# Optimization experiments

Measured on AMD Instinct MI355X. Metric: run time of the kernel, lower is better.

The kernel has to match this reference:

```python
import jax, jax.numpy as jnp
import numpy as np

B, S, D, H = 2, 512, 1024, 8
DK = D // H
DFF = 4 * D
R = 51
SEP = 64


def setup_inputs() -> dict:
    key = jax.random.key(0)
    ks = jax.random.split(key, 12)
    def w(k, shape, scale=0.02):
        return jax.random.normal(k, shape, jnp.float32) * scale
    return {
        "x": jax.random.normal(ks[0], (B, S, D), jnp.float32),
        "relation": jax.random.randint(ks[1], (B, S, S), 0, R),
        "mask": jnp.ones((B, S, S), jnp.int32),
        "sep_id": SEP,
        "history_reg": jnp.ones((1,), jnp.float32),
        "Wq": w(ks[2], (D, D)), "bq": jnp.zeros((D,), jnp.float32),
        "Wk": w(ks[3], (D, D)), "bk": jnp.zeros((D,), jnp.float32),
        "Wv": w(ks[4], (D, D)), "bv": jnp.zeros((D,), jnp.float32),
        "Wo": w(ks[5], (D, D)), "bo": jnp.zeros((D,), jnp.float32),
        "rel_k_emb": w(ks[6], (R, DK)),
        "rel_v_emb": w(ks[7], (R, DK)),
        "ln1_g": jnp.ones((D,), jnp.float32), "ln1_b": jnp.zeros((D,), jnp.float32),
        "ln2_g": jnp.ones((D,), jnp.float32), "ln2_b": jnp.zeros((D,), jnp.float32),
        "W1": w(ks[8], (D, DFF)), "b1": jnp.zeros((DFF,), jnp.float32),
        "W2": w(ks[9], (DFF, D)), "b2": jnp.zeros((D,), jnp.float32),
    }


def _layer_norm(x, g, b, eps=1e-5):
    m = jnp.mean(x, axis=-1, keepdims=True)
    v = jnp.mean(jnp.square(x - m), axis=-1, keepdims=True)
    return (x - m) * jax.lax.rsqrt(v + eps) * g + b


def _forward(x, relation, mask, sep_id, history_reg, Wq, bq, Wk, bk, Wv, bv, Wo, bo,
             rel_k_emb, rel_v_emb, ln1_g, ln1_b, ln2_g, ln2_b, W1, b1, W2, b2):
    b, s, d = x.shape
    # relation-aware self-attention sublayer (pre-norm)
    h = _layer_norm(x, ln1_g, ln1_b)
    rk = rel_k_emb[relation]  # [B,S,S,DK]
    rv = rel_v_emb[relation]  # [B,S,S,DK]
    def proj(W, bias):
        return (h @ W + bias).reshape(b, s, H, DK).transpose(0, 2, 1, 3)  # [B,H,S,DK]
    q, k, v = proj(Wq, bq), proj(Wk, bk), proj(Wv, bv)
    scores = jnp.einsum("bhid,bhjd->bhij", q, k) + jnp.einsum("bhid,bijd->bhij", q, rk)
    scores = scores / jnp.sqrt(jnp.float32(DK))
    scores = jnp.where(mask[:, None, :, :] == 0, jnp.float32(-1e9), scores)
    attn = jax.nn.softmax(scores, axis=-1)  # [B,H,S,S]
    ctx = jnp.einsum("bhij,bhjd->bhid", attn, v) + jnp.einsum("bhij,bijd->bhid", attn, rv)
    ctx = ctx.transpose(0, 2, 1, 3).reshape(b, s, d)
    attn_out = ctx @ Wo + bo
    # history regularization loss: attention mass on history tokens (positions < sep_id)
    loss = history_reg[0] * jnp.mean(attn[:, :, :, :sep_id])
    x = x + attn_out
    # FFN sublayer (pre-norm)
    h2 = _layer_norm(x, ln2_g, ln2_b)
    ffn = jax.nn.relu(h2 @ W1 + b1) @ W2 + b2
    x = x + ffn
    return x, loss


def reference(x, relation, mask, sep_id, history_reg, Wq, bq, Wk, bk, Wv, bv, Wo, bo,
              rel_k_emb, rel_v_emb, ln1_g, ln1_b, ln2_g, ln2_b, W1, b1, W2, b2):
    return _forward(x, relation, mask, sep_id, history_reg, Wq, bq, Wk, bk, Wv, bv,
                    Wo, bo, rel_k_emb, rel_v_emb, ln1_g, ln1_b, ln2_g, ln2_b,
                    W1, b1, W2, b2)
```

## Files before the change

### kernel.cpp

```cpp
#include <hip/hip_runtime.h>
#include <hip/hip_bf16.h>

#define NB 2
#define NS 512
#define ND 1024
#define NH 8
#define NDK 128
#define NDFF 4096
#define RPAD 64
#define BSROWS 1024
#define NBH 16
#define QT 16
#define SLB 536

typedef __bf16 bf16x8 __attribute__((ext_vector_type(8)));
typedef __bf16 bf16x4 __attribute__((ext_vector_type(4)));
typedef float f32x4 __attribute__((ext_vector_type(4)));

#define BM 64
#define BN 64
#define BK 64

__device__ __forceinline__ void gload16(const void* g, void* l) {
    __builtin_amdgcn_global_load_lds(
        (const __attribute__((address_space(1))) void*)g,
        (__attribute__((address_space(3))) void*)l, 16, 0, 0);
}

__global__ __launch_bounds__(256, 4) void gemm64(
    const __bf16* __restrict__ A, const __bf16* __restrict__ Bt,
    __bf16* __restrict__ vt,
    float* __restrict__ Cf, __bf16* __restrict__ Cb,
    const float* __restrict__ bias,
    int Ksp, int lda, int ldb, int ldc,
    long sA, long sA2, int zdivA,
    long sB, long sB2, int zdivB,
    long sC, int nsplit, long sPart, int flags)
{
    __shared__ __bf16 As0[BM * BK];
    __shared__ __bf16 As1[BM * BK];
    __shared__ __bf16 Bs0[BN * BK];
    __shared__ __bf16 Bs1[BN * BK];

    const unsigned gx = gridDim.x, gy = gridDim.y;
    const unsigned n = gx * gy * gridDim.z;
    const unsigned o = blockIdx.x + gx * (blockIdx.y + gy * blockIdx.z);
    const unsigned q = n >> 3, r = n & 7, xcd = o & 7;
    const unsigned nl = (xcd < r ? xcd * (q + 1) : r * (q + 1) + (xcd - r) * q) + (o >> 3);
    const unsigned bx = nl % gx, tmp = nl / gx;
    const unsigned by = tmp % gy, bz = tmp / gy;

    const int z = bz;
    const int bh = z / nsplit, sp = z - bh * nsplit;
    const long kbase = (long)sp * Ksp;
    A  += (long)(bh / zdivA) * sA + (long)(bh % zdivA) * sA2 + kbase;
    Bt += (long)(bh / zdivB) * sB + (long)(bh % zdivB) * sB2 + kbase;
    const long cbase = (long)bh * sC + (long)sp * sPart;

    const int tM = by * BM, tN = bx * BN;
    const int t = threadIdx.x, lane = t & 63, w = t >> 6;
    const int wr = w >> 1, wc = w & 1;

    const int srow = lane >> 3;
    const int scolE = ((((lane & 7) << 4) ^ (srow << 4)) >> 1);

    const __bf16* gA = A + (long)(tM + srow) * lda + scolE;
    const __bf16* gB = Bt + (long)(tN + srow) * ldb + scolE;

    f32x4 acc[2][2];
#pragma unroll
    for (int m = 0; m < 2; ++m)
#pragma unroll
        for (int nn = 0; nn < 2; ++nn)
#pragma unroll
            for (int j = 0; j < 4; ++j) acc[m][nn][j] = 0.f;

    const int r16 = lane & 15;
    const int kq = (lane >> 4) * 8;
    const int xorE = (r16 & 7) * 8;
    const int nt = Ksp / BK;

    auto STAGE = [&](__bf16* as, __bf16* bs, int k0) {
#pragma unroll
        for (int i = 0; i < 2; ++i) {
            const int rr = (w + i * 4) * 8;
            gload16(gA + (long)rr * lda + k0, (void*)&as[rr * BK]);
            gload16(gB + (long)rr * ldb + k0, (void*)&bs[rr * BK]);
        }
    };
    auto COMPUTE = [&](const __bf16* as, const __bf16* bs) {
        __builtin_amdgcn_s_setprio(1);
#pragma unroll
        for (int ks = 0; ks < 2; ++ks) {
            bf16x8 af[2], bv[2];
#pragma unroll
            for (int m = 0; m < 2; ++m)
                af[m] = *(const bf16x8*)&as[(wr * 32 + m * 16 + r16) * BK + ((ks * 32 + kq) ^ xorE)];
#pragma unroll
            for (int nn = 0; nn < 2; ++nn)
                bv[nn] = *(const bf16x8*)&bs[(wc * 32 + nn * 16 + r16) * BK + ((ks * 32 + kq) ^ xorE)];
#pragma unroll
            for (int m = 0; m < 2; ++m)
#pragma unroll
                for (int nn = 0; nn < 2; ++nn)
                    acc[m][nn] = __builtin_amdgcn_mfma_f32_16x16x32_bf16(af[m], bv[nn], acc[m][nn], 0, 0, 0);
        }
        __builtin_amdgcn_s_setprio(0);
    };

    STAGE(As0, Bs0, 0);
    STAGE(As1, Bs1, BK);
    for (int tt = 0; tt < nt; tt += 2) {
        asm volatile("s_waitcnt vmcnt(4)\n\ts_barrier" ::: "memory");
        COMPUTE(As0, Bs0);
        asm volatile("s_waitcnt lgkmcnt(0)\n\ts_barrier" ::: "memory");
        const bool more = (tt + 2 < nt);
        if (more) {
            STAGE(As0, Bs0, (tt + 2) * BK);
            asm volatile("s_waitcnt vmcnt(4)\n\ts_barrier" ::: "memory");
        } else {
            asm volatile("s_waitcnt vmcnt(0)\n\ts_barrier" ::: "memory");
        }
        COMPUTE(As1, Bs1);
        asm volatile("s_waitcnt lgkmcnt(0)\n\ts_barrier" ::: "memory");
        if (more) STAGE(As1, Bs1, (tt + 3) * BK);
    }

    const bool relu = (flags & 1) != 0;
    const bool vmode = (flags & 8) && (tN >= 2 * ND);
#pragma unroll
    for (int m = 0; m < 2; ++m) {
        const int gr0 = tM + wr * 32 + m * 16 + (lane >> 4) * 4;
#pragma unroll
        for (int nn = 0; nn < 2; ++nn) {
            const int gc = tN + wc * 32 + nn * 16 + (lane & 15);
            const float bb = bias ? bias[gc] : 0.f;
            if (vmode) {
                const int hd = gc - 2 * ND;
                const int b = gr0 >> 9, i = gr0 & 511;
                bf16x4 ov;
#pragma unroll
                for (int j = 0; j < 4; ++j) ov[j] = (__bf16)(acc[m][nn][j] + bb);
                *(bf16x4*)&vt[(((long)b * NH + (hd >> 7)) * NDK + (hd & 127)) * NS + i] = ov;
            } else {
#pragma unroll
                for (int j = 0; j < 4; ++j) {
                    float v = acc[m][nn][j] + bb;
                    if (relu) v = fmaxf(v, 0.f);
                    const long idx = cbase + (long)(gr0 + j) * ldc + gc;
                    if (Cb) Cb[idx] = (__bf16)v;
                    else Cf[idx] = v;
                }
            }
        }
    }
}

__global__ __launch_bounds__(256, 2) void attn_fused(
    const __bf16* __restrict__ qkvb, const __bf16* __restrict__ vt,
    const __bf16* __restrict__ relkT, const __bf16* __restrict__ relvT,
    const int* __restrict__ relation, const int* __restrict__ mask,
    __bf16* __restrict__ ctxm, float* __restrict__ loss_part,
    const int* __restrict__ sep_p)
{
    __shared__ __bf16 Sl[QT * SLB];
    __shared__ __bf16 Ks0[64 * NDK];
    __shared__ __bf16 Ks1[64 * NDK];
    __shared__ float qrl[QT][RPAD];
    __shared__ float bins[QT][68];
    __shared__ float redl[4];

    const unsigned o = blockIdx.x + 32u * blockIdx.y;
    const unsigned nl = (o & 7) * 64u + (o >> 3);
    const int qt = nl & 31, bh = nl >> 5;
    const int b = bh >> 3, h = bh & 7;
    const int i0 = qt * QT;

    const int t = threadIdx.x, lane = t & 63, w = t >> 6;
    const int r16 = lane & 15;
    const int kq = (lane >> 4) * 8;
    const int xorE = (r16 & 7) * 8;
    const int sep = *sep_p;

    bf16x8 qf[4];
    {
        const __bf16* qrow = qkvb + ((long)(b * NS + i0 + r16)) * (3 * ND) + h * NDK;
#pragma unroll
        for (int ks = 0; ks < 4; ++ks)
            qf[ks] = *(const bf16x8*)(qrow + ks * 32 + kq);
    }

    int4 ra[4][2], ma[4][2];
#pragma unroll
    for (int rr = 0; rr < 4; ++rr) {
        const long rg = (long)(b * NS + i0 + w * 4 + rr) * NS;
        ra[rr][0] = ((const int4*)(relation + rg))[lane * 2];
        ra[rr][1] = ((const int4*)(relation + rg))[lane * 2 + 1];
        ma[rr][0] = ((const int4*)(mask + rg))[lane * 2];
        ma[rr][1] = ((const int4*)(mask + rg))[lane * 2 + 1];
    }

    {
        f32x4 a;
#pragma unroll
        for (int j = 0; j < 4; ++j) a[j] = 0.f;
#pragma unroll
        for (int ks = 0; ks < 4; ++ks) {
            const bf16x8 bfr = *(const bf16x8*)(relkT + (long)(w * 16 + r16) * NDK + ks * 32 + kq);
            a = __builtin_amdgcn_mfma_f32_16x16x32_bf16(qf[ks], bfr, a, 0, 0, 0);
        }
#pragma unroll
        for (int j = 0; j < 4; ++j)
            qrl[(lane >> 4) * 4 + j][w * 16 + (lane & 15)] = a[j];
    }
    for (int idx = t; idx < QT * 68; idx += 256) ((float*)bins)[idx] = 0.f;

    auto KSTAGE = [&](__bf16* ksb, int kv0) {
#pragma unroll
        for (int ii = 0; ii < 4; ++ii) {
            const int Lc = (w * 4 + ii) * 64 + lane;
            const int j = Lc >> 4, cc = Lc & 15;
            gload16(qkvb + ((long)(b * NS + kv0 + j)) * (3 * ND) + ND + h * NDK + ((cc ^ (j & 7)) << 3),
                    (void*)&ksb[(w * 4 + ii) * 512]);
        }
    };
    auto SCOMP = [&](const __bf16* ksb, int kv0) {
        f32x4 s;
#pragma unroll
        for (int j = 0; j < 4; ++j) s[j] = 0.f;
#pragma unroll
        for (int ks = 0; ks < 4; ++ks) {
            const bf16x8 bfr = *(const bf16x8*)&ksb[(w * 16 + r16) * NDK + ((ks * 32 + kq) ^ xorE)];
            s = __builtin_amdgcn_mfma_f32_16x16x32_bf16(qf[ks], bfr, s, 0, 0, 0);
        }
        const int colb = kv0 + w * 16 + (lane & 15);
#pragma unroll
        for (int j = 0; j < 4; ++j)
            Sl[((lane >> 4) * 4 + j) * SLB + colb] = (__bf16)s[j];
    };

    KSTAGE(Ks0, 0);
    KSTAGE(Ks1, 64);
    for (int tt = 0; tt < 8; tt += 2) {
        asm volatile("s_waitcnt vmcnt(4)\n\ts_barrier" ::: "memory");
        SCOMP(Ks0, tt * 64);
        asm volatile("s_waitcnt lgkmcnt(0)\n\ts_barrier" ::: "memory");
        const bool more = (tt + 2 < 8);
        if (more) {
            KSTAGE(Ks0, (tt + 2) * 64);
            asm volatile("s_waitcnt vmcnt(4)\n\ts_barrier" ::: "memory");
        } else {
            asm volatile("s_waitcnt vmcnt(0)\n\ts_barrier" ::: "memory");
        }
        SCOMP(Ks1, (tt + 1) * 64);
        asm volatile("s_waitcnt lgkmcnt(0)\n\ts_barrier" ::: "memory");
        if (more) KSTAGE(Ks1, (tt + 3) * 64);
    }

    const int brow = t & 15;
    const int bj0 = (t >> 4) * 32;
    int4 br[8];
    {
        const int4* rp = (const int4*)(relation + ((long)(b * NS + i0 + brow)) * NS + bj0);
#pragma unroll
        for (int c = 0; c < 8; ++c) br[c] = rp[c];
    }

    auto VSTAGE = [&](__bf16* vs, int kv0) {
#pragma unroll
        for (int ii = 0; ii < 4; ++ii) {
            const int d = w * 32 + ii * 8 + (lane >> 3);
            const int cc = lane & 7;
            gload16(vt + ((long)bh * NDK + d) * NS + kv0 + ((cc ^ (d & 7)) << 3),
                    (void*)&vs[(w * 32 + ii * 8) * 64]);
        }
    };
    VSTAGE(Ks0, 0);
    VSTAGE(Ks1, 64);

    const float sc = 0.088388347648318447f;
    float lsum = 0.f;
#pragma unroll
    for (int rr = 0; rr < 4; ++rr) {
        const int row = w * 4 + rr;
        const bf16x8 sv = *(const bf16x8*)&Sl[row * SLB + lane * 8];
        int rl[8], mm[8];
        rl[0] = ra[rr][0].x; rl[1] = ra[rr][0].y; rl[2] = ra[rr][0].z; rl[3] = ra[rr][0].w;
        rl[4] = ra[rr][1].x; rl[5] = ra[rr][1].y; rl[6] = ra[rr][1].z; rl[7] = ra[rr][1].w;
        mm[0] = ma[rr][0].x; mm[1] = ma[rr][0].y; mm[2] = ma[rr][0].z; mm[3] = ma[rr][0].w;
        mm[4] = ma[rr][1].x; mm[5] = ma[rr][1].y; mm[6] = ma[rr][1].z; mm[7] = ma[rr][1].w;
        float v[8];
        float mx = -1e30f;
#pragma unroll
        for (int q = 0; q < 8; ++q) {
            float vv = ((float)sv[q] + qrl[row][rl[q]]) * sc;
            if (mm[q] == 0) vv = -1e9f;
            v[q] = vv;
            mx = fmaxf(mx, vv);
        }
#pragma unroll
        for (int of = 32; of > 0; of >>= 1) mx = fmaxf(mx, __shfl_xor(mx, of, 64));
        float sm = 0.f;
#pragma unroll
        for (int q = 0; q < 8; ++q) { v[q] = __expf(v[q] - mx); sm += v[q]; }
#pragma unroll
        for (int of = 32; of > 0; of >>= 1) sm += __shfl_xor(sm, of, 64);
        const float inv = 1.f / sm;
        bf16x8 av;
#pragma unroll
        for (int q = 0; q < 8; ++q) {
            const float a = v[q] * inv;
            av[q] = (__bf16)a;
            if (lane * 8 + q < sep) lsum += a;
        }
        *(bf16x8*)&Sl[row * SLB + lane * 8] = av;
    }
#pragma unroll
    for (int of = 32; of > 0; of >>= 1) lsum += __shfl_xor(lsum, of, 64);
    if (lane == 0) redl[w] = lsum;
    asm volatile("s_waitcnt lgkmcnt(0)\n\ts_barrier" ::: "memory");
    if (t == 0) loss_part[bh * 32 + qt] = redl[0] + redl[1] + redl[2] + redl[3];

    {
        const __bf16* ap = &Sl[brow * SLB + bj0];
#pragma unroll
        for (int c = 0; c < 8; ++c) {
            const bf16x4 a4 = *(const bf16x4*)(ap + c * 4);
            atomicAdd(&bins[brow][br[c].x], (float)a4[0]);
            atomicAdd(&bins[brow][br[c].y], (float)a4[1]);
            atomicAdd(&bins[brow][br[c].z], (float)a4[2]);
            atomicAdd(&bins[brow][br[c].w], (float)a4[3]);
        }
    }

    f32x4 oacc[2];
#pragma unroll
    for (int nn = 0; nn < 2; ++nn)
#pragma unroll
        for (int j = 0; j < 4; ++j) oacc[nn][j] = 0.f;

    auto PVCOMP = [&](const __bf16* vs, int kv0) {
        __builtin_amdgcn_s_setprio(1);
#pragma unroll
        for (int ks = 0; ks < 2; ++ks) {
            const bf16x8 af = *(const bf16x8*)&Sl[r16 * SLB + kv0 + ks * 32 + kq];
#pragma unroll
            for (int nn = 0; nn < 2; ++nn) {
                const bf16x8 bv = *(const bf16x8*)&vs[(w * 32 + nn * 16 + r16) * 64 + ((ks * 32 + kq) ^ xorE)];
                oacc[nn] = __builtin_amdgcn_mfma_f32_16x16x32_bf16(af, bv, oacc[nn], 0, 0, 0);
            }
        }
        __builtin_amdgcn_s_setprio(0);
    };

    for (int tt = 0; tt < 8; tt += 2) {
        asm volatile("s_waitcnt vmcnt(4)\n\ts_barrier" ::: "memory");
        PVCOMP(Ks0, tt * 64);
        asm volatile("s_waitcnt lgkmcnt(0)\n\ts_barrier" ::: "memory");
        const bool more = (tt + 2 < 8);
        if (more) {
            VSTAGE(Ks0, (tt + 2) * 64);
            asm volatile("s_waitcnt vmcnt(4)\n\ts_barrier" ::: "memory");
        } else {
            asm volatile("s_waitcnt vmcnt(0)\n\ts_barrier" ::: "memory");
        }
        PVCOMP(Ks1, (tt + 1) * 64);
        asm volatile("s_waitcnt lgkmcnt(0)\n\ts_barrier" ::: "memory");
        if (more) VSTAGE(Ks1, (tt + 3) * 64);
    }

#pragma unroll
    for (int kc = 0; kc < 2; ++kc) {
        const float4 b0 = *(const float4*)&bins[r16][kc * 32 + kq];
        const float4 b1 = *(const float4*)&bins[r16][kc * 32 + kq + 4];
        bf16x8 af;
        af[0] = (__bf16)b0.x; af[1] = (__bf16)b0.y; af[2] = (__bf16)b0.z; af[3] = (__bf16)b0.w;
        af[4] = (__bf16)b1.x; af[5] = (__bf16)b1.y; af[6] = (__bf16)b1.z; af[7] = (__bf16)b1.w;
#pragma unroll
        for (int nn = 0; nn < 2; ++nn) {
            const bf16x8 bfr = *(const bf16x8*)(relvT + (long)(w * 32 + nn * 16 + r16) * RPAD + kc * 32 + kq);
            oacc[nn] = __builtin_amdgcn_mfma_f32_16x16x32_bf16(af, bfr, oacc[nn], 0, 0, 0);
        }
    }
#pragma unroll
    for (int nn = 0; nn < 2; ++nn)
#pragma unroll
        for (int j = 0; j < 4; ++j) {
            const int row = (lane >> 4) * 4 + j;
            ctxm[((long)(b * NS + i0 + row)) * ND + h * NDK + w * 32 + nn * 16 + (lane & 15)] =
                (__bf16)oacc[nn][j];
        }
}

__global__ void prep_weights(
    const float* __restrict__ Wq, const float* __restrict__ Wk,
    const float* __restrict__ Wv, const float* __restrict__ Wo,
    const float* __restrict__ W1, const float* __restrict__ W2,
    const float* __restrict__ relv,
    const float* __restrict__ bq, const float* __restrict__ bk,
    const float* __restrict__ bv, const float* __restrict__ relk,
    const float* __restrict__ x, const float* __restrict__ ln1g,
    const float* __restrict__ ln1b,
    __bf16* __restrict__ WqkvT, __bf16* __restrict__ WoT,
    __bf16* __restrict__ W1T, __bf16* __restrict__ W2T,
    __bf16* __restrict__ relvT, float* __restrict__ biasqkv,
    __bf16* __restrict__ relkT, __bf16* __restrict__ h1, int R)
{
    const int tile = blockIdx.x;
    const int t = threadIdx.y * 32 + threadIdx.x;

    if (tile >= 12372) {
        const long row = tile - 12372;
        const float* xr = x + row * ND;
        float4 v = reinterpret_cast<const float4*>(xr)[t];
        float s = v.x + v.y + v.z + v.w;
        float s2 = v.x * v.x + v.y * v.y + v.z * v.z + v.w * v.w;
#pragma unroll
        for (int o = 32; o > 0; o >>= 1) {
            s += __shfl_xor(s, o, 64);
            s2 += __shfl_xor(s2, o, 64);
        }
        __shared__ float red[8];
        const int lane = t & 63, wv = t >> 6;
        if (lane == 0) { red[wv] = s; red[4 + wv] = s2; }
        __syncthreads();
        s = red[0] + red[1] + red[2] + red[3];
        s2 = red[4] + red[5] + red[6] + red[7];
        const float mean = s * (1.f / ND);
        const float var = s2 * (1.f / ND) - mean * mean;
        const float rs = rsqrtf(var + 1e-5f);
        const float xv[4] = {v.x, v.y, v.z, v.w};
        bf16x4 o;
#pragma unroll
        for (int j = 0; j < 4; ++j) {
            const int c = t * 4 + j;
            o[j] = (__bf16)((xv[j] - mean) * rs * ln1g[c] + ln1b[c]);
        }
        *(bf16x4*)&h1[row * ND + t * 4] = o;
        return;
    }
    if (tile >= 12296) {
        const int ft = (tile - 12296) * 256 + t;
        if (ft < ND) biasqkv[ft] = bq[ft];
        else if (ft < 2 * ND) biasqkv[ft] = bk[ft - ND];
        else if (ft < 3 * ND) biasqkv[ft] = bv[ft - 2 * ND];
        else {
            const int idx = ft - 3 * ND;
            if (idx < 128 * NDK) {
                const int r = idx / NDK;
                relkT[idx] = (r < R) ? (__bf16)relk[idx] : (__bf16)0.f;
            }
        }
        return;
    }
    const float* src; __bf16* dst;
    int rows_in, cols_in, ldo, kx, ny;
    if (tile < 4096) {
        const int m = tile >> 10, r = tile & 1023;
        kx = r & 31; ny = r >> 5;
        rows_in = 1024; cols_in = 1024; ldo = 1024;
        src = m == 0 ? Wq : m == 1 ? Wk : m == 2 ? Wv : Wo;
        dst = m == 3 ? WoT : WqkvT + (size_t)m * 1024 * 1024;
    } else if (tile < 8192) {
        const int r = tile - 4096;
        kx = r & 31; ny = r >> 5;
        rows_in = 1024; cols_in = 4096; ldo = 1024; src = W1; dst = W1T;
    } else if (tile < 12288) {
        const int r = tile - 8192;
        kx = r & 127; ny = r >> 7;
        rows_in = 4096; cols_in = 1024; ldo = 4096; src = W2; dst = W2T;
    } else {
        const int r = tile - 12288;
        kx = r & 1; ny = r >> 1;
        rows_in = R; cols_in = 128; ldo = 64; src = relv; dst = relvT;
    }

    __shared__ float tl[32][33];
    const int k0 = kx * 32, n0 = ny * 32;
    const int tx = threadIdx.x, ty = threadIdx.y;
#pragma unroll
    for (int dy = 0; dy < 32; dy += 8) {
        const int k = k0 + ty + dy, nn = n0 + tx;
        tl[ty + dy][tx] = (k < rows_in && nn < cols_in) ? src[(long)k * cols_in + nn] : 0.f;
    }
    __syncthreads();
#pragma unroll
    for (int dy = 0; dy < 32; dy += 8) {
        const int nn = n0 + ty + dy, k = k0 + tx;
        if (nn < cols_in && k < ldo) dst[(long)nn * ldo + k] = (__bf16)tl[tx][ty + dy];
    }
}

__global__ __launch_bounds__(256) void wo_reduce_ln(
    const float* __restrict__ P, const float* __restrict__ x,
    const float* __restrict__ bo, const float* __restrict__ g,
    const float* __restrict__ bb, float* __restrict__ out,
    __bf16* __restrict__ h2)
{
    const int row = blockIdx.x;
    const int t = threadIdx.x;
    const long i4 = (long)row * 256 + t;
    const long sP = (long)BSROWS * ND / 4;
    const float4* P4 = (const float4*)P;
    float4 s = P4[i4];
    const float4 t1 = P4[i4 + sP];
    s.x += t1.x; s.y += t1.y; s.z += t1.z; s.w += t1.w;
    const int col = t * 4;
    const float4 xv = ((const float4*)x)[i4];
    const float4 bv = *(const float4*)&bo[col];
    float4 o;
    o.x = s.x + xv.x + bv.x; o.y = s.y + xv.y + bv.y;
    o.z = s.z + xv.z + bv.z; o.w = s.w + xv.w + bv.w;
    ((float4*)out)[i4] = o;

    float sum = o.x + o.y + o.z + o.w;
    float sum2 = o.x * o.x + o.y * o.y + o.z * o.z + o.w * o.w;
#pragma unroll
    for (int of = 32; of > 0; of >>= 1) {
        sum += __shfl_xor(sum, of, 64);
        sum2 += __shfl_xor(sum2, of, 64);
    }
    __shared__ float red[8];
    const int lane = t & 63, wv = t >> 6;
    if (lane == 0) { red[wv] = sum; red[4 + wv] = sum2; }
    __syncthreads();
    sum = red[0] + red[1] + red[2] + red[3];
    sum2 = red[4] + red[5] + red[6] + red[7];
    const float mean = sum * (1.f / ND);
    const float var = sum2 * (1.f / ND) - mean * mean;
    const float rs = rsqrtf(var + 1e-5f);
    const float ov[4] = {o.x, o.y, o.z, o.w};
    bf16x4 hb;
#pragma unroll
    for (int j = 0; j < 4; ++j)
        hb[j] = (__bf16)((ov[j] - mean) * rs * g[col + j] + bb[col + j]);
    *(bf16x4*)&h2[(long)row * ND + col] = hb;
}

__global__ __launch_bounds__(256) void ffn2_reduce(
    const float* __restrict__ P, const float* __restrict__ b2, float* __restrict__ out,
    const float* __restrict__ loss_part, const float* __restrict__ hist,
    const int* __restrict__ sep_p, float* __restrict__ out_loss)
{
    const int i4 = blockIdx.x * 256 + threadIdx.x;
    const long sP = (long)BSROWS * ND / 4;
    const float4* P4 = (const float4*)P;
    float4 s = P4[i4];
    const float4 t1 = P4[i4 + sP];
    s.x += t1.x; s.y += t1.y; s.z += t1.z; s.w += t1.w;
    const int col = (i4 * 4) & (ND - 1);
    const float4 bv = *(const float4*)&b2[col];
    float4 o = ((float4*)out)[i4];
    o.x += s.x + bv.x; o.y += s.y + bv.y;
    o.z += s.z + bv.z; o.w += s.w + bv.w;
    ((float4*)out)[i4] = o;

    if (blockIdx.x == 0) {
        const int t = threadIdx.x;
        float ls = 0.f;
        if (t < 128) {
            const float4 v = ((const float4*)loss_part)[t];
            ls = v.x + v.y + v.z + v.w;
        }
#pragma unroll
        for (int of = 32; of > 0; of >>= 1) ls += __shfl_xor(ls, of, 64);
        __shared__ float red[4];
        if ((t & 63) == 0) red[t >> 6] = ls;
        __syncthreads();
        if (t == 0) {
            const int sep = *sep_p;
            const float total = red[0] + red[1] + red[2] + red[3];
            const float denom = (float)NB * NH * NS * (float)(sep > 0 ? sep : 1);
            out_loss[0] = (sep > 0) ? hist[0] * total / denom : 0.f;
        }
    }
}

extern "C" void kernel_launch(void* const* d_in, const int* in_sizes, int n_in,
                              void* d_out, int out_size, void* d_ws, size_t ws_size,
                              hipStream_t stream)
{
    const float* x      = (const float*)d_in[0];
    const int* relation = (const int*)d_in[1];
    const int* mask     = (const int*)d_in[2];
    const int* sep_p    = (const int*)d_in[3];
    const float* hist   = (const float*)d_in[4];
    const float* Wq = (const float*)d_in[5],  *bq = (const float*)d_in[6];
    const float* Wk = (const float*)d_in[7],  *bk = (const float*)d_in[8];
    const float* Wv = (const float*)d_in[9],  *bv = (const float*)d_in[10];
    const float* Wo = (const float*)d_in[11], *bo = (const float*)d_in[12];
    const float* relk = (const float*)d_in[13];
    const float* relv = (const float*)d_in[14];
    const float* ln1g = (const float*)d_in[15], *ln1b = (const float*)d_in[16];
    const float* ln2g = (const float*)d_in[17], *ln2b = (const float*)d_in[18];
    const float* W1 = (const float*)d_in[19], *b1 = (const float*)d_in[20];
    const float* W2 = (const float*)d_in[21], *b2 = (const float*)d_in[22];
    const int R = in_sizes[13] / NDK;

    float* out = (float*)d_out;
    float* out_loss = out + (long)BSROWS * ND;

    char* p = (char*)d_ws;
    auto alloc = [&](size_t bytes) -> void* {
        void* r = (void*)p;
        p += (bytes + 255) & ~(size_t)255;
        return r;
    };
    __bf16* WqkvT   = (__bf16*)alloc((size_t)3 * ND * ND * 2);
    __bf16* WoT     = (__bf16*)alloc((size_t)ND * ND * 2);
    __bf16* W1T     = (__bf16*)alloc((size_t)NDFF * ND * 2);
    __bf16* W2T     = (__bf16*)alloc((size_t)ND * NDFF * 2);
    __bf16* relkT   = (__bf16*)alloc((size_t)128 * NDK * 2);
    __bf16* relvT   = (__bf16*)alloc((size_t)NDK * RPAD * 2);
    float*  biasqkv = (float*)alloc((size_t)3 * ND * 4);
    __bf16* h1      = (__bf16*)alloc((size_t)BSROWS * ND * 2);
    __bf16* qkvb    = (__bf16*)alloc((size_t)BSROWS * 3 * ND * 2);
    __bf16* vt      = (__bf16*)alloc((size_t)NBH * NDK * NS * 2);
    __bf16* ctxm    = (__bf16*)alloc((size_t)BSROWS * ND * 2);
    __bf16* h2      = (__bf16*)alloc((size_t)BSROWS * ND * 2);
    __bf16* F1      = (__bf16*)alloc((size_t)BSROWS * NDFF * 2);
    float*  loss_part = (float*)alloc((size_t)512 * 4);
    float*  arena   = (float*)alloc((size_t)16 * 1024 * 1024);
    float* woPart   = arena;
    float* f2Part   = arena + (size_t)2 * 1024 * 1024;

    const dim3 tb(32, 8);
    prep_weights<<<13396, tb, 0, stream>>>(Wq, Wk, Wv, Wo, W1, W2, relv,
                                           bq, bk, bv, relk, x, ln1g, ln1b,
                                           WqkvT, WoT, W1T, W2T, relvT,
                                           biasqkv, relkT, h1, R);

    gemm64<<<dim3(48, 16, 1), 256, 0, stream>>>(
        h1, WqkvT, vt, nullptr, qkvb, biasqkv,
        ND, ND, ND, 3 * ND,
        0, 0, 1, 0, 0, 1, 0, 1, 0, 8);

    attn_fused<<<dim3(32, 16), 256, 0, stream>>>(
        qkvb, vt, relkT, relvT, relation, mask, ctxm, loss_part, sep_p);

    gemm64<<<dim3(16, 16, 2), 256, 0, stream>>>(
        ctxm, WoT, nullptr, woPart, nullptr, nullptr,
        512, ND, ND, ND,
        0, 0, 1, 0, 0, 1,
        0, 2, (long)BSROWS * ND, 0);

    wo_reduce_ln<<<BSROWS, 256, 0, stream>>>(woPart, x, bo, ln2g, ln2b, out, h2);

    gemm64<<<dim3(64, 16, 1), 256, 0, stream>>>(
        h2, W1T, nullptr, nullptr, F1, b1,
        ND, ND, ND, NDFF,
        0, 0, 1, 0, 0, 1, 0, 1, 0, 1);

    gemm64<<<dim3(16, 16, 2), 256, 0, stream>>>(
        F1, W2T, nullptr, f2Part, nullptr, nullptr,
        2048, NDFF, NDFF, ND,
        0, 0, 1, 0, 0, 1,
        0, 2, (long)BSROWS * ND, 0);

    ffn2_reduce<<<1024, 256, 0, stream>>>(f2Part, b2, out,
                                          loss_part, hist, sep_p, out_loss);
}
```

Baseline: 131.6 us.

## Halve attention query tile to 8 rows and single-buffer K/V staging for occupancy

Shrinks the attention query tile from 16 to 8 rows, so twice as many blocks are launched (1024). K and V staging drops from double to single buffering to cut LDS use, and launch bounds are raised to 4 waves per SIMD. The aim is more resident blocks to hide latency. The cost is that half the MFMA rows are wasted on padding, K/V tiles are reloaded twice as often overall, and the prefetch overlap between load and compute is lost.

```diff
diff --git a/kernel.cpp b/kernel.cpp
--- a/kernel.cpp
+++ b/kernel.cpp
@@ -10,7 +10,7 @@
 #define RPAD 64
 #define BSROWS 1024
 #define NBH 16
-#define QT 16
+#define QT 8
 #define SLB 536
 
 typedef __bf16 bf16x8 __attribute__((ext_vector_type(8)));
@@ -156,7 +156,7 @@
     }
 }
 
-__global__ __launch_bounds__(256, 2) void attn_fused(
+__global__ __launch_bounds__(256, 4) void attn_fused(
     const __bf16* __restrict__ qkvb, const __bf16* __restrict__ vt,
     const __bf16* __restrict__ relkT, const __bf16* __restrict__ relvT,
     const int* __restrict__ relation, const int* __restrict__ mask,
@@ -164,42 +164,51 @@
     const int* __restrict__ sep_p)
 {
     __shared__ __bf16 Sl[QT * SLB];
-    __shared__ __bf16 Ks0[64 * NDK];
-    __shared__ __bf16 Ks1[64 * NDK];
+    __shared__ __bf16 Ks[64 * NDK];
     __shared__ float qrl[QT][RPAD];
     __shared__ float bins[QT][68];
     __shared__ float redl[4];
 
-    const unsigned o = blockIdx.x + 32u * blockIdx.y;
-    const unsigned nl = (o & 7) * 64u + (o >> 3);
-    const int qt = nl & 31, bh = nl >> 5;
+    const unsigned o = blockIdx.x + 64u * blockIdx.y;
+    const unsigned nl = (o & 7) * 128u + (o >> 3);
+    const int qt = nl & 63, bh = nl >> 6;
     const int b = bh >> 3, h = bh & 7;
     const int i0 = qt * QT;
 
     const int t = threadIdx.x, lane = t & 63, w = t >> 6;
     const int r16 = lane & 15;
+    const int r8 = r16 & 7;
     const int kq = (lane >> 4) * 8;
-    const int xorE = (r16 & 7) * 8;
+    const int xorE = r8 * 8;
     const int sep = *sep_p;
 
     bf16x8 qf[4];
     {
-        const __bf16* qrow = qkvb + ((long)(b * NS + i0 + r16)) * (3 * ND) + h * NDK;
+        const __bf16* qrow = qkvb + ((long)(b * NS + i0 + r8)) * (3 * ND) + h * NDK;
 #pragma unroll
         for (int ks = 0; ks < 4; ++ks)
             qf[ks] = *(const bf16x8*)(qrow + ks * 32 + kq);
     }
 
-    int4 ra[4][2], ma[4][2];
-#pragma unroll
-    for (int rr = 0; rr < 4; ++rr) {
-        const long rg = (long)(b * NS + i0 + w * 4 + rr) * NS;
+    int4 ra[2][2], ma[2][2];
+#pragma unroll
+    for (int rr = 0; rr < 2; ++rr) {
+        const long rg = (long)(b * NS + i0 + w * 2 + rr) * NS;
         ra[rr][0] = ((const int4*)(relation + rg))[lane * 2];
         ra[rr][1] = ((const int4*)(relation + rg))[lane * 2 + 1];
         ma[rr][0] = ((const int4*)(mask + rg))[lane * 2];
         ma[rr][1] = ((const int4*)(mask + rg))[lane * 2 + 1];
     }
 
+    const int brow = t & 7;
+    const int bj0 = (t >> 3) * 16;
+    int4 br[4];
+    {
+        const int4* rp = (const int4*)(relation + ((long)(b * NS + i0 + brow)) * NS + bj0);
+#pragma unroll
+        for (int c = 0; c < 4; ++c) br[c] = rp[c];
+    }
+
     {
         f32x4 a;
 #pragma unroll
@@ -210,79 +219,51 @@
             a = __builtin_amdgcn_mfma_f32_16x16x32_bf16(qf[ks], bfr, a, 0, 0, 0);
         }
 #pragma unroll
-        for (int j = 0; j < 4; ++j)
-            qrl[(lane >> 4) * 4 + j][w * 16 + (lane & 15)] = a[j];
+        for (int j = 0; j < 4; ++j) {
+            const int row = (lane >> 4) * 4 + j;
+            if (row < QT) qrl[row][w * 16 + (lane & 15)] = a[j];
+        }
     }
     for (int idx = t; idx < QT * 68; idx += 256) ((float*)bins)[idx] = 0.f;
 
-    auto KSTAGE = [&](__bf16* ksb, int kv0) {
+    auto KSTAGE = [&](int kv0) {
 #pragma unroll
         for (int ii = 0; ii < 4; ++ii) {
             const int Lc = (w * 4 + ii) * 64 + lane;
             const int j = Lc >> 4, cc = Lc & 15;
             gload16(qkvb + ((long)(b * NS + kv0 + j)) * (3 * ND) + ND + h * NDK + ((cc ^ (j & 7)) << 3),
-                    (void*)&ksb[(w * 4 + ii) * 512]);
+                    (void*)&Ks[(w * 4 + ii) * 512]);
         }
     };
-    auto SCOMP = [&](const __bf16* ksb, int kv0) {
+    auto SCOMP = [&](int kv0) {
         f32x4 s;
 #pragma unroll
         for (int j = 0; j < 4; ++j) s[j] = 0.f;
 #pragma unroll
         for (int ks = 0; ks < 4; ++ks) {
-            const bf16x8 bfr = *(const bf16x8*)&ksb[(w * 16 + r16) * NDK + ((ks * 32 + kq) ^ xorE)];
+            const bf16x8 bfr = *(const bf16x8*)&Ks[(w * 16 + r16) * NDK + ((ks * 32 + kq) ^ xorE)];
             s = __builtin_amdgcn_mfma_f32_16x16x32_bf16(qf[ks], bfr, s, 0, 0, 0);
         }
         const int colb = kv0 + w * 16 + (lane & 15);
 #pragma unroll
-        for (int j = 0; j < 4; ++j)
-            Sl[((lane >> 4) * 4 + j) * SLB + colb] = (__bf16)s[j];
+        for (int j = 0; j < 4; ++j) {
+            const int row = (lane >> 4) * 4 + j;
+            if (row < QT) Sl[row * SLB + colb] = (__bf16)s[j];
+        }
     };
 
-    KSTAGE(Ks0, 0);
-    KSTAGE(Ks1, 64);
-    for (int tt = 0; tt < 8; tt += 2) {
-        asm volatile("s_waitcnt vmcnt(4)\n\ts_barrier" ::: "memory");
-        SCOMP(Ks0, tt * 64);
+    for (int tt = 0; tt < 8; ++tt) {
+        KSTAGE(tt * 64);
+        asm volatile("s_waitcnt vmcnt(0)\n\ts_barrier" ::: "memory");
+        SCOMP(tt * 64);
         asm volatile("s_waitcnt lgkmcnt(0)\n\ts_barrier" ::: "memory");
-        const bool more = (tt + 2 < 8);
-        if (more) {
-            KSTAGE(Ks0, (tt + 2) * 64);
-            asm volatile("s_waitcnt vmcnt(4)\n\ts_barrier" ::: "memory");
-        } else {
-            asm volatile("s_waitcnt vmcnt(0)\n\ts_barrier" ::: "memory");
-        }
-        SCOMP(Ks1, (tt + 1) * 64);
-        asm volatile("s_waitcnt lgkmcnt(0)\n\ts_barrier" ::: "memory");
-        if (more) KSTAGE(Ks1, (tt + 3) * 64);
-    }
-
-    const int brow = t & 15;
-    const int bj0 = (t >> 4) * 32;
-    int4 br[8];
-    {
-        const int4* rp = (const int4*)(relation + ((long)(b * NS + i0 + brow)) * NS + bj0);
-#pragma unroll
-        for (int c = 0; c < 8; ++c) br[c] = rp[c];
-    }
-
-    auto VSTAGE = [&](__bf16* vs, int kv0) {
-#pragma unroll
-        for (int ii = 0; ii < 4; ++ii) {
-            const int d = w * 32 + ii * 8 + (lane >> 3);
-            const int cc = lane & 7;
-            gload16(vt + ((long)bh * NDK + d) * NS + kv0 + ((cc ^ (d & 7)) << 3),
-                    (void*)&vs[(w * 32 + ii * 8) * 64]);
-        }
-    };
-    VSTAGE(Ks0, 0);
-    VSTAGE(Ks1, 64);
+    }
 
     const float sc = 0.088388347648318447f;
     float lsum = 0.f;
 #pragma unroll
-    for (int rr = 0; rr < 4; ++rr) {
-        const int row = w * 4 + rr;
+    for (int rr = 0; rr < 2; ++rr) {
+        const int row = w * 2 + rr;
         const bf16x8 sv = *(const bf16x8*)&Sl[row * SLB + lane * 8];
         int rl[8], mm[8];
         rl[0] = ra[rr][0].x; rl[1] = ra[rr][0].y; rl[2] = ra[rr][0].z; rl[3] = ra[rr][0].w;
@@ -319,12 +300,12 @@
     for (int of = 32; of > 0; of >>= 1) lsum += __shfl_xor(lsum, of, 64);
     if (lane == 0) redl[w] = lsum;
     asm volatile("s_waitcnt lgkmcnt(0)\n\ts_barrier" ::: "memory");
-    if (t == 0) loss_part[bh * 32 + qt] = redl[0] + redl[1] + redl[2] + redl[3];
+    if (t == 0) loss_part[bh * 64 + qt] = redl[0] + redl[1] + redl[2] + redl[3];
 
     {
         const __bf16* ap = &Sl[brow * SLB + bj0];
 #pragma unroll
-        for (int c = 0; c < 8; ++c) {
+        for (int c = 0; c < 4; ++c) {
             const bf16x4 a4 = *(const bf16x4*)(ap + c * 4);
             atomicAdd(&bins[brow][br[c].x], (float)a4[0]);
             atomicAdd(&bins[brow][br[c].y], (float)a4[1]);
@@ -339,40 +320,40 @@
 #pragma unroll
         for (int j = 0; j < 4; ++j) oacc[nn][j] = 0.f;
 
-    auto PVCOMP = [&](const __bf16* vs, int kv0) {
+    auto VSTAGE = [&](int kv0) {
+#pragma unroll
+        for (int ii = 0; ii < 4; ++ii) {
+            const int d = w * 32 + ii * 8 + (lane >> 3);
+            const int cc = lane & 7;
+            gload16(vt + ((long)bh * NDK + d) * NS + kv0 + ((cc ^ (d & 7)) << 3),
+                    (void*)&Ks[(w * 32 + ii * 8) * 64]);
+        }
+    };
+    auto PVCOMP = [&](int kv0) {
         __builtin_amdgcn_s_setprio(1);
 #pragma unroll
         for (int ks = 0; ks < 2; ++ks) {
-            const bf16x8 af = *(const bf16x8*)&Sl[r16 * SLB + kv0 + ks * 32 + kq];
+            const bf16x8 af = *(const bf16x8*)&Sl[r8 * SLB + kv0 + ks * 32 + kq];
 #pragma unroll
             for (int nn = 0; nn < 2; ++nn) {
-                const bf16x8 bv = *(const bf16x8*)&vs[(w * 32 + nn * 16 + r16) * 64 + ((ks * 32 + kq) ^ xorE)];
+                const bf16x8 bv = *(const bf16x8*)&Ks[(w * 32 + nn * 16 + r16) * 64 + ((ks * 32 + kq) ^ xorE)];
                 oacc[nn] = __builtin_amdgcn_mfma_f32_16x16x32_bf16(af, bv, oacc[nn], 0, 0, 0);
             }
         }
         __builtin_amdgcn_s_setprio(0);
     };
 
-    for (int tt = 0; tt < 8; tt += 2) {
-        asm volatile("s_waitcnt vmcnt(4)\n\ts_barrier" ::: "memory");
-        PVCOMP(Ks0, tt * 64);
+    for (int tt = 0; tt < 8; ++tt) {
+        VSTAGE(tt * 64);
+        asm volatile("s_waitcnt vmcnt(0)\n\ts_barrier" ::: "memory");
+        PVCOMP(tt * 64);
         asm volatile("s_waitcnt lgkmcnt(0)\n\ts_barrier" ::: "memory");
-        const bool more = (tt + 2 < 8);
-        if (more) {
-            VSTAGE(Ks0, (tt + 2) * 64);
-            asm volatile("s_waitcnt vmcnt(4)\n\ts_barrier" ::: "memory");
-        } else {
-            asm volatile("s_waitcnt vmcnt(0)\n\ts_barrier" ::: "memory");
-        }
-        PVCOMP(Ks1, (tt + 1) * 64);
-        asm volatile("s_waitcnt lgkmcnt(0)\n\ts_barrier" ::: "memory");
-        if (more) VSTAGE(Ks1, (tt + 3) * 64);
     }
 
 #pragma unroll
     for (int kc = 0; kc < 2; ++kc) {
-        const float4 b0 = *(const float4*)&bins[r16][kc * 32 + kq];
-        const float4 b1 = *(const float4*)&bins[r16][kc * 32 + kq + 4];
+        const float4 b0 = *(const float4*)&bins[r8][kc * 32 + kq];
+        const float4 b1 = *(const float4*)&bins[r8][kc * 32 + kq + 4];
         bf16x8 af;
         af[0] = (__bf16)b0.x; af[1] = (__bf16)b0.y; af[2] = (__bf16)b0.z; af[3] = (__bf16)b0.w;
         af[4] = (__bf16)b1.x; af[5] = (__bf16)b1.y; af[6] = (__bf16)b1.z; af[7] = (__bf16)b1.w;
@@ -387,8 +368,9 @@
 #pragma unroll
         for (int j = 0; j < 4; ++j) {
             const int row = (lane >> 4) * 4 + j;
-            ctxm[((long)(b * NS + i0 + row)) * ND + h * NDK + w * 32 + nn * 16 + (lane & 15)] =
-                (__bf16)oacc[nn][j];
+            if (row < QT)
+                ctxm[((long)(b * NS + i0 + row)) * ND + h * NDK + w * 32 + nn * 16 + (lane & 15)] =
+                    (__bf16)oacc[nn][j];
         }
 }
 
@@ -557,11 +539,8 @@
 
     if (blockIdx.x == 0) {
         const int t = threadIdx.x;
-        float ls = 0.f;
-        if (t < 128) {
-            const float4 v = ((const float4*)loss_part)[t];
-            ls = v.x + v.y + v.z + v.w;
-        }
+        const float4 v = ((const float4*)loss_part)[t];
+        float ls = v.x + v.y + v.z + v.w;
 #pragma unroll
         for (int of = 32; of > 0; of >>= 1) ls += __shfl_xor(ls, of, 64);
         __shared__ float red[4];
@@ -619,7 +598,7 @@
     __bf16* ctxm    = (__bf16*)alloc((size_t)BSROWS * ND * 2);
     __bf16* h2      = (__bf16*)alloc((size_t)BSROWS * ND * 2);
     __bf16* F1      = (__bf16*)alloc((size_t)BSROWS * NDFF * 2);
-    float*  loss_part = (float*)alloc((size_t)512 * 4);
+    float*  loss_part = (float*)alloc((size_t)1024 * 4);
     float*  arena   = (float*)alloc((size_t)16 * 1024 * 1024);
     float* woPart   = arena;
     float* f2Part   = arena + (size_t)2 * 1024 * 1024;
@@ -635,7 +614,7 @@
         ND, ND, ND, 3 * ND,
         0, 0, 1, 0, 0, 1, 0, 1, 0, 8);
 
-    attn_fused<<<dim3(32, 16), 256, 0, stream>>>(
+    attn_fused<<<dim3(64, 16), 256, 0, stream>>>(
         qkvb, vt, relkT, relvT, relation, mask, ctxm, loss_part, sep_p);
 
     gemm64<<<dim3(16, 16, 2), 256, 0, stream>>>(
```

New measurement: 136.6 us. +3.8%, slower.
